# Kernel tuning notes

Hardware: AMD Instinct MI355X
Metric: run time of the kernel (lower is better)

Reference implementation:

```python
import jax, jax.numpy as jnp
import numpy as np

NUM_HEADS = 16

def setup_inputs() -> dict:
    key = jax.random.key(0)
    ks = jax.random.split(key, 8)
    B, S, D = 2, 2048, 1024
    H = NUM_HEADS
    s = 0.02
    return {
        "x": jax.random.normal(ks[0], (B, S, D), jnp.float32),
        "Wqkv": jax.random.normal(ks[1], (D, 3 * D), jnp.float32) * s,
        "bqkv": jnp.zeros((3 * D,), jnp.float32),
        "Wo": jax.random.normal(ks[2], (D, D), jnp.float32) * s,
        "bo": jnp.zeros((D,), jnp.float32),
        "mobius_scale": jnp.full((H,), 0.1, jnp.float32),
        "W1": jax.random.normal(ks[3], (D, D // 2), jnp.float32) * s,
        "b1": jnp.zeros((D // 2,), jnp.float32),
        "W2": jax.random.normal(ks[4], (D // 2, H), jnp.float32) * s,
        "b2": jnp.zeros((H,), jnp.float32),
        "adaptive_weight": jnp.full((1,), 0.1, jnp.float32),
    }

def reference(x, Wqkv, bqkv, Wo, bo, mobius_scale, W1, b1, W2, b2, adaptive_weight):
    B, S, D = x.shape
    H = NUM_HEADS
    dh = D // H
    # --- adaptive gating MLP on pooled context ---
    context = jnp.mean(x, axis=1, keepdims=True)                      # (B,1,D)
    h = jax.nn.gelu(context @ W1 + b1, approximate=False)             # (B,1,D/2)
    adaptive_factors = jax.nn.sigmoid(h @ W2 + b2)                    # (B,1,H)
    # --- incidence attention with mobius term ---
    qkv = (x @ Wqkv + bqkv).reshape(B, S, 3, H, dh)
    q, k, v = qkv[:, :, 0], qkv[:, :, 1], qkv[:, :, 2]                # (B,S,H,dh)
    scores = jnp.einsum("bshd,bthd->bhst", q, k) / jnp.sqrt(jnp.float32(dh))
    # Mobius map of the raw scores, learnable per-head scale
    scores = scores + mobius_scale[None, :, None, None] * (scores / (1.0 + scores * scores))
    attn = jax.nn.softmax(scores, axis=-1)                            # (B,H,S,S)
    out = jnp.einsum("bhst,bthd->bshd", attn, v).reshape(B, S, D)
    base_output = out @ Wo + bo                                       # (B,S,D)
    # --- training-path elementwise rescale ---
    adjustment = jnp.mean(adaptive_factors, axis=-1, keepdims=True)   # (B,1,1)
    return base_output * (1.0 + adaptive_weight * adjustment)
```

## Files before the change

kernel.cpp:

```cpp
#include <hip/hip_runtime.h>
#include <hip/hip_bf16.h>
#include <stdint.h>

typedef unsigned short u16;
typedef unsigned int u32;
typedef __attribute__((ext_vector_type(8))) short short8;
typedef __attribute__((ext_vector_type(4))) float f32x4;
typedef __attribute__((ext_vector_type(2))) float f32x2;
typedef __attribute__((ext_vector_type(4))) unsigned short u16x4;
typedef __attribute__((ext_vector_type(2))) unsigned int u32x2;

#define DEVFN static __device__ __forceinline__


DEVFN u16 f2bf(float f) {
  u32 u = __float_as_uint(f);
  u = (u + 0x7FFFu + ((u >> 16) & 1u)) >> 16;
  return (u16)u;
}

DEVFN u32 cvtpk_bf16(float lo, float hi) {
  u32 r;
  asm("v_cvt_pk_bf16_f32 %0, %1, %2" : "=v"(r) : "v"(lo), "v"(hi));
  return r;
}

DEVFN void gll16(const void* g, void* l) {
  __builtin_amdgcn_global_load_lds((const __attribute__((address_space(1))) u32*)g,
                                   (__attribute__((address_space(3))) u32*)l, 16, 0, 0);
}


__global__ void ctx_partial_kernel(const float* __restrict__ x, float* __restrict__ ctx) {
  int blk = blockIdx.x;
  int b = blk >> 7;
  int s0 = (blk & 127) * 16;
  int t = threadIdx.x;
  const float* xb = x + (size_t)b * 2048 * 1024 + (size_t)s0 * 1024;
#pragma unroll
  for (int c = 0; c < 4; ++c) {
    int d = c * 256 + t;
    float sum = 0.f;
#pragma unroll
    for (int s = 0; s < 16; ++s) sum += xb[(size_t)s * 1024 + d];
    atomicAdd(&ctx[b * 1024 + d], sum);
  }
}

__global__ void adaptive1_kernel(const float* __restrict__ ctx, const float* __restrict__ W1,
                                 const float* __restrict__ b1, float* __restrict__ hbuf) {
  int b = blockIdx.x >> 3, jb = blockIdx.x & 7;
  int t = threadIdx.x;
  int j = jb * 64 + (t & 63);
  int part = t >> 6;
  __shared__ float ctxs[1024];
  __shared__ float partial[4][64];
  for (int i = t; i < 1024; i += 256) ctxs[i] = ctx[b * 1024 + i] * (1.0f / 2048.0f);
  __syncthreads();
  float a0 = 0.f, a1 = 0.f;
  int d0 = part * 256;
  for (int d = d0; d < d0 + 256; d += 2) {
    a0 += ctxs[d] * W1[(size_t)d * 512 + j];
    a1 += ctxs[d + 1] * W1[(size_t)(d + 1) * 512 + j];
  }
  partial[part][t & 63] = a0 + a1;
  __syncthreads();
  if (t < 64) {
    float acc = b1[j] + ((partial[0][t] + partial[1][t]) + (partial[2][t] + partial[3][t]));
    hbuf[b * 512 + j] = 0.5f * acc * (1.0f + erff(acc * 0.70710678118654752f));
  }
}

__global__ void adaptive2_kernel(const float* __restrict__ hbuf, const float* __restrict__ W2,
                                 const float* __restrict__ b2, const float* __restrict__ aw,
                                 float* __restrict__ scale) {
  int b = blockIdx.x;
  int t = threadIdx.x;
  __shared__ float part[256];
  int o = t & 15, seg = t >> 4;
  float a = 0.f;
  for (int j = seg * 32; j < seg * 32 + 32; ++j) a += hbuf[b * 512 + j] * W2[(size_t)j * 16 + o];
  part[t] = a;
  __syncthreads();
  if (t < 16) {
    float acc = b2[t];
    for (int s2 = 0; s2 < 16; ++s2) acc += part[s2 * 16 + t];
    part[t] = 1.0f / (1.0f + __expf(-acc));
  }
  __syncthreads();
  if (t == 0) {
    float s = 0.f;
    for (int i = 0; i < 16; ++i) s += part[i];
    scale[b] = 1.0f + aw[0] * (s * (1.0f / 16.0f));
  }
}


__global__ void cvt_bf16_kernel(const float* __restrict__ in, u16* __restrict__ out, int n4) {
  int i = blockIdx.x * blockDim.x + threadIdx.x;
  if (i < n4) {
    float4 v = ((const float4*)in)[i];
    u16x4 o = {f2bf(v.x), f2bf(v.y), f2bf(v.z), f2bf(v.w)};
    ((u16x4*)out)[i] = o;
  }
}

__global__ void transpose_bf16_kernel(const float* __restrict__ in, u16* __restrict__ out,
                                      int K, int N) {
  __shared__ u16 tile[32][33];
  int n0 = blockIdx.x * 32, k0 = blockIdx.y * 32;
  int tc = threadIdx.x & 31, tr = threadIdx.x >> 5;
  for (int i = tr; i < 32; i += 8)
    tile[i][tc] = f2bf(in[(size_t)(k0 + i) * N + n0 + tc]);
  __syncthreads();
  for (int i = tr; i < 32; i += 8)
    out[(size_t)(n0 + i) * K + k0 + tc] = tile[tc][i];
}


DEVFN void gemm_tile_mainloop(const u16* __restrict__ A, const u16* __restrict__ Bt,
                              int m0, int n0, int K, u16* As, u16* Bs, f32x4 acc[4][4]) {
  const int tid = threadIdx.x;
  const int lane = tid & 63, wid = tid >> 6;
  const int wr = wid >> 1, wc = wid & 1;
  const int lr = lane & 15, lg = lane >> 4;
  const int srow = tid >> 2;
  const int scol = ((tid & 3) ^ ((tid >> 3) & 3)) * 8;
  const int axor = ((lr >> 1) & 3) << 4;

  const u16* ag0 = A + (size_t)(m0 + srow) * K + scol;
  const u16* ag1 = ag0 + (size_t)64 * K;
  const u16* bg0 = Bt + (size_t)(n0 + srow) * K + scol;
  const u16* bg1 = bg0 + (size_t)64 * K;

  gll16(ag0, As + tid * 8);
  gll16(ag1, As + (tid + 256) * 8);
  gll16(bg0, Bs + tid * 8);
  gll16(bg1, Bs + (tid + 256) * 8);

  int cur = 0;
  for (int k0 = 0; k0 < K; k0 += 32) {
    __syncthreads();
    if (k0 + 32 < K) {
      int nb = (cur ^ 1) * 4096;
      gll16(ag0 + k0 + 32, As + nb + tid * 8);
      gll16(ag1 + k0 + 32, As + nb + (tid + 256) * 8);
      gll16(bg0 + k0 + 32, Bs + nb + tid * 8);
      gll16(bg1 + k0 + 32, Bs + nb + (tid + 256) * 8);
    }
    const char* Ac = (const char*)(As + cur * 4096);
    const char* Bc = (const char*)(Bs + cur * 4096);
    short8 af[4], bf[4];
#pragma unroll
    for (int i = 0; i < 4; ++i)
      af[i] = *(const short8*)(Ac + (wr * 64 + i * 16 + lr) * 64 + ((lg * 16) ^ axor));
#pragma unroll
    for (int j = 0; j < 4; ++j)
      bf[j] = *(const short8*)(Bc + (wc * 64 + j * 16 + lr) * 64 + ((lg * 16) ^ axor));
#pragma unroll
    for (int i = 0; i < 4; ++i)
#pragma unroll
      for (int j = 0; j < 4; ++j)
        acc[i][j] = __builtin_amdgcn_mfma_f32_16x16x32_bf16(af[i], bf[j], acc[i][j], 0, 0, 0);
    cur ^= 1;
  }
}

DEVFN void gemm64_mainloop(const u16* __restrict__ A, const u16* __restrict__ Bt,
                           int m0, int n0, int K, u16* As, u16* Bs, f32x4 acc[2][2]) {
  const int tid = threadIdx.x;
  const int lane = tid & 63, wid = tid >> 6;
  const int wr = wid >> 1, wc = wid & 1;
  const int lr = lane & 15, lg = lane >> 4;
  const int srow = tid >> 2;
  const int scol = ((tid & 3) ^ ((tid >> 3) & 3)) * 8;
  const int axor = ((lr >> 1) & 3) << 4;

  const u16* ag = A + (size_t)(m0 + srow) * K + scol;
  const u16* bg = Bt + (size_t)(n0 + srow) * K + scol;
  gll16(ag, As + tid * 8);
  gll16(bg, Bs + tid * 8);

  int cur = 0;
  for (int k0 = 0; k0 < K; k0 += 32) {
    __syncthreads();
    if (k0 + 32 < K) {
      int nb = (cur ^ 1) * 2048;
      gll16(ag + k0 + 32, As + nb + tid * 8);
      gll16(bg + k0 + 32, Bs + nb + tid * 8);
    }
    const char* Ac = (const char*)(As + cur * 2048);
    const char* Bc = (const char*)(Bs + cur * 2048);
    short8 af[2], bf[2];
#pragma unroll
    for (int i = 0; i < 2; ++i)
      af[i] = *(const short8*)(Ac + (wr * 32 + i * 16 + lr) * 64 + ((lg * 16) ^ axor));
#pragma unroll
    for (int j = 0; j < 2; ++j)
      bf[j] = *(const short8*)(Bc + (wc * 32 + j * 16 + lr) * 64 + ((lg * 16) ^ axor));
#pragma unroll
    for (int i = 0; i < 2; ++i)
#pragma unroll
      for (int j = 0; j < 2; ++j)
        acc[i][j] = __builtin_amdgcn_mfma_f32_16x16x32_bf16(af[i], bf[j], acc[i][j], 0, 0, 0);
    cur ^= 1;
  }
}

__global__ __launch_bounds__(256) void gemm_qkv_kernel(
    const u16* __restrict__ A, const u16* __restrict__ Bt, const float* __restrict__ bias,
    u16* __restrict__ Qb, u16* __restrict__ Kb, u16* __restrict__ Vt) {
  __shared__ __align__(16) u16 As[2 * 128 * 32];
  __shared__ __align__(16) u16 Bs[2 * 128 * 32];
  f32x4 acc[4][4];
  const f32x4 z = {0.f, 0.f, 0.f, 0.f};
#pragma unroll
  for (int i = 0; i < 4; ++i)
#pragma unroll
    for (int j = 0; j < 4; ++j) acc[i][j] = z;
  int m0 = blockIdx.y * 128, n0 = blockIdx.x * 128;
  gemm_tile_mainloop(A, Bt, m0, n0, 1024, As, Bs, acc);

  const int lane = threadIdx.x & 63, wid = threadIdx.x >> 6;
  const int wr = wid >> 1, wc = wid & 1, lr = lane & 15, lg = lane >> 4;
#pragma unroll
  for (int j = 0; j < 4; ++j) {
    int col = n0 + wc * 64 + j * 16 + lr;
    float bv = bias[col];
    int c3 = col >> 10;
    int hh = (col >> 6) & 15, dd = col & 63;
    float qs = (c3 == 0) ? 0.125f : 1.0f;
#pragma unroll
    for (int i = 0; i < 4; ++i) {
      int row0 = m0 + wr * 64 + i * 16 + lg * 4;
      if (c3 == 2) {
        int b = row0 >> 11, s0 = row0 & 2047;
        u16x4 pv = {f2bf(acc[i][j][0] + bv), f2bf(acc[i][j][1] + bv),
                    f2bf(acc[i][j][2] + bv), f2bf(acc[i][j][3] + bv)};
        *(u16x4*)&Vt[(((size_t)b * 16 + hh) * 64 + dd) * 2048 + s0] = pv;
      } else {
        u16* dst = (c3 == 0) ? Qb : Kb;
#pragma unroll
        for (int r = 0; r < 4; ++r)
          dst[(size_t)(row0 + r) * 1024 + (col & 1023)] = f2bf((acc[i][j][r] + bv) * qs);
      }
    }
  }
}

__global__ __launch_bounds__(256) void gemm_out_kernel(
    const u16* __restrict__ A, const u16* __restrict__ Bt, const float* __restrict__ bo,
    const float* __restrict__ scale, float* __restrict__ out) {
  __shared__ __align__(16) u16 As[2 * 64 * 32];
  __shared__ __align__(16) u16 Bs[2 * 64 * 32];
  f32x4 acc[2][2];
  const f32x4 z = {0.f, 0.f, 0.f, 0.f};
#pragma unroll
  for (int i = 0; i < 2; ++i)
#pragma unroll
    for (int j = 0; j < 2; ++j) acc[i][j] = z;
  int m0 = blockIdx.y * 64, n0 = blockIdx.x * 64;
  gemm64_mainloop(A, Bt, m0, n0, 1024, As, Bs, acc);

  const int lane = threadIdx.x & 63, wid = threadIdx.x >> 6;
  const int wr = wid >> 1, wc = wid & 1, lr = lane & 15, lg = lane >> 4;
#pragma unroll
  for (int j = 0; j < 2; ++j) {
    int col = n0 + wc * 32 + j * 16 + lr;
    float bv = bo[col];
#pragma unroll
    for (int i = 0; i < 2; ++i) {
      int row0 = m0 + wr * 32 + i * 16 + lg * 4;
      float sc = scale[row0 >> 11];
#pragma unroll
      for (int r = 0; r < 4; ++r)
        out[(size_t)(row0 + r) * 1024 + col] = (acc[i][j][r] + bv) * sc;
    }
  }
}

__global__ __launch_bounds__(256) void attn_kernel(
    const u16* __restrict__ Qb, const u16* __restrict__ Kb, const u16* __restrict__ Vt,
    const float* __restrict__ mobius, u16* __restrict__ O) {
  __shared__ __align__(16) u16 Ks[2][64 * 64];
  __shared__ __align__(16) u16 Vs[2][64 * 64];
  __shared__ __align__(16) u16 Ps[64 * 64];
  const int tid = threadIdx.x;
  const int lane = tid & 63, w = tid >> 6;
  const int lr = lane & 15, lg = lane >> 4;
  const int bid = blockIdx.x;
  const int bidx = (bid & 7) * 128 + (bid >> 3);
  const int qb = bidx & 31, h = (bidx >> 5) & 15, b = bidx >> 9;
  const float msc = mobius[h];

  const int srow = tid >> 3;
  const int scol = ((tid & 7) ^ (srow & 7)) * 8;
  const int rxor = (lr & 7) << 4;

  const u16* qgl =
      Qb + (size_t)(b * 2048 + qb * 64 + w * 16 + lr) * 1024 + h * 64 + lg * 8;
  short8 qf0 = *(const short8*)qgl;
  short8 qf1 = *(const short8*)(qgl + 32);

  const u16* kg = Kb + (size_t)(b * 2048 + srow) * 1024 + h * 64 + scol;
  const u16* vg = Vt + ((size_t)(b * 16 + h) * 64 + srow) * 2048 + scol;

  gll16(kg, Ks[0] + tid * 8);
  gll16(kg + (size_t)32 * 1024, Ks[0] + (tid + 256) * 8);
  gll16(vg, Vs[0] + tid * 8);
  gll16(vg + 32 * 2048, Vs[0] + (tid + 256) * 8);

  float m_run = -3.0e38f, l_run = 0.0f;
  f32x4 acc_o[4];
  const f32x4 z = {0.f, 0.f, 0.f, 0.f};
#pragma unroll
  for (int i = 0; i < 4; ++i) acc_o[i] = z;

  const f32x2 one2 = {1.0f, 1.0f};
  const f32x2 msc2 = {msc, msc};
  const int qrow = w * 16 + lr;
  int cur = 0;
  for (int kt = 0; kt < 32; ++kt) {
    __syncthreads();
    if (kt < 31) {
      const u16* kgn = kg + (size_t)(kt + 1) * 64 * 1024;
      const u16* vgn = vg + (kt + 1) * 64;
      u16* Kn = Ks[cur ^ 1];
      u16* Vn = Vs[cur ^ 1];
      gll16(kgn, Kn + tid * 8);
      gll16(kgn + (size_t)32 * 1024, Kn + (tid + 256) * 8);
      gll16(vgn, Vn + tid * 8);
      gll16(vgn + 32 * 2048, Vn + (tid + 256) * 8);
    }
    const char* Kc = (const char*)Ks[cur];
    const char* Vc = (const char*)Vs[cur];
    const char* Pc = (const char*)Ps;

    f32x4 sacc[4];
#pragma unroll
    for (int i = 0; i < 4; ++i) sacc[i] = z;
    {
      int cbx = (lg * 16) ^ rxor;
#pragma unroll
      for (int ki = 0; ki < 4; ++ki) {
        short8 kf = *(const short8*)(Kc + (ki * 16 + lr) * 128 + cbx);
        sacc[ki] = __builtin_amdgcn_mfma_f32_16x16x32_bf16(kf, qf0, sacc[ki], 0, 0, 0);
      }
      cbx = (64 + lg * 16) ^ rxor;
#pragma unroll
      for (int ki = 0; ki < 4; ++ki) {
        short8 kf = *(const short8*)(Kc + (ki * 16 + lr) * 128 + cbx);
        sacc[ki] = __builtin_amdgcn_mfma_f32_16x16x32_bf16(kf, qf1, sacc[ki], 0, 0, 0);
      }
    }

    f32x2 p2[8];
    f32x2 mx = {-3.0e38f, -3.0e38f};
#pragma unroll
    for (int i = 0; i < 8; ++i) {
      int ki = i >> 1, jj = i & 1;
      f32x2 s = {sacc[ki][jj * 2], sacc[ki][jj * 2 + 1]};
      f32x2 d = s * s + one2;
      f32x2 rr = {__builtin_amdgcn_rcpf(d.x), __builtin_amdgcn_rcpf(d.y)};
      f32x2 t = msc2 * (s * rr) + s;
      p2[i] = t;
      mx = __builtin_elementwise_max(mx, t);
    }
    float tmax = fmaxf(mx.x, mx.y);
    tmax = fmaxf(tmax, __shfl_xor(tmax, 16));
    tmax = fmaxf(tmax, __shfl_xor(tmax, 32));
    float m_new = fmaxf(m_run, tmax);
    float corr = __expf(m_run - m_new);
    f32x2 m2 = {m_new, m_new};
    f32x2 sum2 = {0.f, 0.f};
#pragma unroll
    for (int i = 0; i < 8; ++i) {
      f32x2 e = p2[i] - m2;
      f32x2 pe = {__expf(e.x), __expf(e.y)};
      p2[i] = pe;
      sum2 += pe;
    }
    float tsum = sum2.x + sum2.y;
    tsum += __shfl_xor(tsum, 16);
    tsum += __shfl_xor(tsum, 32);
    l_run = l_run * corr + tsum;
    m_run = m_new;

#pragma unroll
    for (int ki = 0; ki < 4; ++ki) {
      u32x2 pw = {cvtpk_bf16(p2[2 * ki].x, p2[2 * ki].y),
                  cvtpk_bf16(p2[2 * ki + 1].x, p2[2 * ki + 1].y)};
      *(u32x2*)(Pc + qrow * 128 + ((ki * 32 + lg * 8) ^ rxor)) = pw;
    }

    float c4[4];
#pragma unroll
    for (int r = 0; r < 4; ++r) c4[r] = __shfl(corr, lg * 4 + r);
#pragma unroll
    for (int di = 0; di < 4; ++di)
#pragma unroll
      for (int r = 0; r < 4; ++r) acc_o[di][r] *= c4[r];

#pragma unroll
    for (int ks = 0; ks < 2; ++ks) {
      int cbx = (ks * 64 + lg * 16) ^ rxor;
      short8 pf = *(const short8*)(Pc + qrow * 128 + cbx);
#pragma unroll
      for (int di = 0; di < 4; ++di) {
        short8 vf = *(const short8*)(Vc + (di * 16 + lr) * 128 + cbx);
        acc_o[di] = __builtin_amdgcn_mfma_f32_16x16x32_bf16(pf, vf, acc_o[di], 0, 0, 0);
      }
    }
    cur ^= 1;
  }

  float linv = 1.0f / l_run;
  float li[4];
#pragma unroll
  for (int r = 0; r < 4; ++r) li[r] = __shfl(linv, lg * 4 + r);
  size_t obase = (size_t)(b * 2048 + qb * 64 + w * 16) * 1024 + h * 64;
#pragma unroll
  for (int di = 0; di < 4; ++di)
#pragma unroll
    for (int r = 0; r < 4; ++r)
      O[obase + (size_t)(lg * 4 + r) * 1024 + di * 16 + lr] = f2bf(acc_o[di][r] * li[r]);
}


extern "C" void kernel_launch(void* const* d_in, const int* in_sizes, int n_in,
                              void* d_out, int out_size, void* d_ws, size_t ws_size,
                              hipStream_t stream) {
  const float* x = (const float*)d_in[0];
  const float* Wqkv = (const float*)d_in[1];
  const float* bqkv = (const float*)d_in[2];
  const float* Wo = (const float*)d_in[3];
  const float* bo = (const float*)d_in[4];
  const float* mob = (const float*)d_in[5];
  const float* W1 = (const float*)d_in[6];
  const float* b1 = (const float*)d_in[7];
  const float* W2 = (const float*)d_in[8];
  const float* b2 = (const float*)d_in[9];
  const float* aw = (const float*)d_in[10];
  float* out = (float*)d_out;

  char* ws = (char*)d_ws;
  float* scale = (float*)ws;
  float* ctx = (float*)(ws + 256);
  float* hbuf = (float*)(ws + 8192);
  u16* xbf = (u16*)(ws + 16384);
  u16* wqkvT = xbf + (size_t)4096 * 1024;
  u16* woT = wqkvT + (size_t)3072 * 1024;
  u16* Qb = woT + (size_t)1024 * 1024;
  u16* Kb = Qb + (size_t)4096 * 1024;
  u16* Vt = Kb + (size_t)4096 * 1024;
  u16* attn = Vt + (size_t)4096 * 1024;

  hipMemsetAsync(ctx, 0, 2048 * sizeof(float), stream);
  ctx_partial_kernel<<<256, 256, 0, stream>>>(x, ctx);
  adaptive1_kernel<<<16, 256, 0, stream>>>(ctx, W1, b1, hbuf);
  adaptive2_kernel<<<2, 256, 0, stream>>>(hbuf, W2, b2, aw, scale);
  cvt_bf16_kernel<<<4096, 256, 0, stream>>>(x, xbf, 1048576);
  transpose_bf16_kernel<<<dim3(96, 32), 256, 0, stream>>>(Wqkv, wqkvT, 1024, 3072);
  transpose_bf16_kernel<<<dim3(32, 32), 256, 0, stream>>>(Wo, woT, 1024, 1024);
  gemm_qkv_kernel<<<dim3(24, 32), 256, 0, stream>>>(xbf, wqkvT, bqkv, Qb, Kb, Vt);
  attn_kernel<<<1024, 256, 0, stream>>>(Qb, Kb, Vt, mob, attn);
  gemm_out_kernel<<<dim3(16, 64), 256, 0, stream>>>(attn, woT, bo, scale, out);
}
```

Baseline: 272.4 us.

## Split attention over keys, fuse x conversion, swizzle GEMM grids, lazy softmax rescale

Attention is split into two key halves, doubling the grid, and a new combine kernel merges the two partial outputs using the saved per-row max and sum. V is read straight from global memory instead of being staged in LDS. The softmax now works in base 2, only rescales when the running max grows by more than a threshold, and raises wave priority around the MFMA sections. The mean-pooling and bf16 conversion of x are fused into one kernel. Both GEMMs get swizzled 1D grids and swapped MFMA operands so their epilogues can issue vectorised stores. The risks are the extra combine pass, the bf16 rounding of partial outputs before merging, and uncached V reads.

```diff
diff --git a/kernel.cpp b/kernel.cpp
--- a/kernel.cpp
+++ b/kernel.cpp
@@ -19,6 +19,8 @@
   return (u16)u;
 }
 
+DEVFN float bf2f(u16 v) { return __uint_as_float((u32)v << 16); }
+
 DEVFN u32 cvtpk_bf16(float lo, float hi) {
   u32 r;
   asm("v_cvt_pk_bf16_f32 %0, %1, %2" : "=v"(r) : "v"(lo), "v"(hi));
@@ -30,21 +32,30 @@
                                    (__attribute__((address_space(3))) u32*)l, 16, 0, 0);
 }
 
-
-__global__ void ctx_partial_kernel(const float* __restrict__ x, float* __restrict__ ctx) {
+__global__ void ctx_cvt_kernel(const float* __restrict__ x, float* __restrict__ ctx,
+                               u16* __restrict__ xbf) {
   int blk = blockIdx.x;
   int b = blk >> 7;
   int s0 = (blk & 127) * 16;
   int t = threadIdx.x;
-  const float* xb = x + (size_t)b * 2048 * 1024 + (size_t)s0 * 1024;
-#pragma unroll
-  for (int c = 0; c < 4; ++c) {
-    int d = c * 256 + t;
-    float sum = 0.f;
-#pragma unroll
-    for (int s = 0; s < 16; ++s) sum += xb[(size_t)s * 1024 + d];
-    atomicAdd(&ctx[b * 1024 + d], sum);
-  }
+  const float* xb = x + ((size_t)b * 2048 + s0) * 1024 + t * 4;
+  u16* ob = xbf + ((size_t)b * 2048 + s0) * 1024 + t * 4;
+  float4 sum = {0.f, 0.f, 0.f, 0.f};
+#pragma unroll
+  for (int s = 0; s < 16; ++s) {
+    float4 v = *(const float4*)(xb + (size_t)s * 1024);
+    sum.x += v.x;
+    sum.y += v.y;
+    sum.z += v.z;
+    sum.w += v.w;
+    u16x4 o = {f2bf(v.x), f2bf(v.y), f2bf(v.z), f2bf(v.w)};
+    *(u16x4*)(ob + (size_t)s * 1024) = o;
+  }
+  float* c = ctx + b * 1024 + t * 4;
+  atomicAdd(c + 0, sum.x);
+  atomicAdd(c + 1, sum.y);
+  atomicAdd(c + 2, sum.z);
+  atomicAdd(c + 3, sum.w);
 }
 
 __global__ void adaptive1_kernel(const float* __restrict__ ctx, const float* __restrict__ W1,
@@ -95,16 +106,6 @@
   }
 }
 
-
-__global__ void cvt_bf16_kernel(const float* __restrict__ in, u16* __restrict__ out, int n4) {
-  int i = blockIdx.x * blockDim.x + threadIdx.x;
-  if (i < n4) {
-    float4 v = ((const float4*)in)[i];
-    u16x4 o = {f2bf(v.x), f2bf(v.y), f2bf(v.z), f2bf(v.w)};
-    ((u16x4*)out)[i] = o;
-  }
-}
-
 __global__ void transpose_bf16_kernel(const float* __restrict__ in, u16* __restrict__ out,
                                       int K, int N) {
   __shared__ u16 tile[32][33];
@@ -161,7 +162,7 @@
     for (int i = 0; i < 4; ++i)
 #pragma unroll
       for (int j = 0; j < 4; ++j)
-        acc[i][j] = __builtin_amdgcn_mfma_f32_16x16x32_bf16(af[i], bf[j], acc[i][j], 0, 0, 0);
+        acc[i][j] = __builtin_amdgcn_mfma_f32_16x16x32_bf16(bf[j], af[i], acc[i][j], 0, 0, 0);
     cur ^= 1;
   }
 }
@@ -202,7 +203,7 @@
     for (int i = 0; i < 2; ++i)
 #pragma unroll
       for (int j = 0; j < 2; ++j)
-        acc[i][j] = __builtin_amdgcn_mfma_f32_16x16x32_bf16(af[i], bf[j], acc[i][j], 0, 0, 0);
+        acc[i][j] = __builtin_amdgcn_mfma_f32_16x16x32_bf16(bf[j], af[i], acc[i][j], 0, 0, 0);
     cur ^= 1;
   }
 }
@@ -218,31 +219,35 @@
   for (int i = 0; i < 4; ++i)
 #pragma unroll
     for (int j = 0; j < 4; ++j) acc[i][j] = z;
-  int m0 = blockIdx.y * 128, n0 = blockIdx.x * 128;
+  int lin = blockIdx.x;
+  int swz = (lin & 7) * 96 + (lin >> 3);
+  int n0 = (swz % 24) * 128, m0 = (swz / 24) * 128;
   gemm_tile_mainloop(A, Bt, m0, n0, 1024, As, Bs, acc);
 
   const int lane = threadIdx.x & 63, wid = threadIdx.x >> 6;
   const int wr = wid >> 1, wc = wid & 1, lr = lane & 15, lg = lane >> 4;
 #pragma unroll
-  for (int j = 0; j < 4; ++j) {
-    int col = n0 + wc * 64 + j * 16 + lr;
-    float bv = bias[col];
-    int c3 = col >> 10;
-    int hh = (col >> 6) & 15, dd = col & 63;
-    float qs = (c3 == 0) ? 0.125f : 1.0f;
-#pragma unroll
-    for (int i = 0; i < 4; ++i) {
-      int row0 = m0 + wr * 64 + i * 16 + lg * 4;
+  for (int i = 0; i < 4; ++i) {
+    int m = m0 + wr * 64 + i * 16 + lr;
+#pragma unroll
+    for (int j = 0; j < 4; ++j) {
+      int nb = n0 + wc * 64 + j * 16 + lg * 4;
+      float4 bv = *(const float4*)&bias[nb];
+      int c3 = nb >> 10;
       if (c3 == 2) {
-        int b = row0 >> 11, s0 = row0 & 2047;
-        u16x4 pv = {f2bf(acc[i][j][0] + bv), f2bf(acc[i][j][1] + bv),
-                    f2bf(acc[i][j][2] + bv), f2bf(acc[i][j][3] + bv)};
-        *(u16x4*)&Vt[(((size_t)b * 16 + hh) * 64 + dd) * 2048 + s0] = pv;
+        int bb = m >> 11, ss = m & 2047;
+        int hh = (nb >> 6) & 15, dd = nb & 63;
+        size_t vb_ = (((size_t)bb * 16 + hh) * 64 + dd) * 2048 + ss;
+        Vt[vb_] = f2bf(acc[i][j][0] + bv.x);
+        Vt[vb_ + 2048] = f2bf(acc[i][j][1] + bv.y);
+        Vt[vb_ + 4096] = f2bf(acc[i][j][2] + bv.z);
+        Vt[vb_ + 6144] = f2bf(acc[i][j][3] + bv.w);
       } else {
         u16* dst = (c3 == 0) ? Qb : Kb;
-#pragma unroll
-        for (int r = 0; r < 4; ++r)
-          dst[(size_t)(row0 + r) * 1024 + (col & 1023)] = f2bf((acc[i][j][r] + bv) * qs);
+        float qs = (c3 == 0) ? 0.125f : 1.0f;
+        u16x4 o = {f2bf((acc[i][j][0] + bv.x) * qs), f2bf((acc[i][j][1] + bv.y) * qs),
+                   f2bf((acc[i][j][2] + bv.z) * qs), f2bf((acc[i][j][3] + bv.w) * qs)};
+        *(u16x4*)&dst[(size_t)m * 1024 + (nb & 1023)] = o;
       }
     }
   }
@@ -259,56 +264,54 @@
   for (int i = 0; i < 2; ++i)
 #pragma unroll
     for (int j = 0; j < 2; ++j) acc[i][j] = z;
-  int m0 = blockIdx.y * 64, n0 = blockIdx.x * 64;
+  int lin = blockIdx.x;
+  int swz = (lin & 7) * 128 + (lin >> 3);
+  int n0 = (swz & 15) * 64, m0 = (swz >> 4) * 64;
   gemm64_mainloop(A, Bt, m0, n0, 1024, As, Bs, acc);
 
   const int lane = threadIdx.x & 63, wid = threadIdx.x >> 6;
   const int wr = wid >> 1, wc = wid & 1, lr = lane & 15, lg = lane >> 4;
 #pragma unroll
-  for (int j = 0; j < 2; ++j) {
-    int col = n0 + wc * 32 + j * 16 + lr;
-    float bv = bo[col];
-#pragma unroll
-    for (int i = 0; i < 2; ++i) {
-      int row0 = m0 + wr * 32 + i * 16 + lg * 4;
-      float sc = scale[row0 >> 11];
-#pragma unroll
-      for (int r = 0; r < 4; ++r)
-        out[(size_t)(row0 + r) * 1024 + col] = (acc[i][j][r] + bv) * sc;
-    }
-  }
-}
-
-__global__ __launch_bounds__(256) void attn_kernel(
+  for (int i = 0; i < 2; ++i) {
+    int m = m0 + wr * 32 + i * 16 + lr;
+    float sc = scale[m >> 11];
+#pragma unroll
+    for (int j = 0; j < 2; ++j) {
+      int nb = n0 + wc * 32 + j * 16 + lg * 4;
+      float4 bv = *(const float4*)&bo[nb];
+      float4 o = {(acc[i][j][0] + bv.x) * sc, (acc[i][j][1] + bv.y) * sc,
+                  (acc[i][j][2] + bv.z) * sc, (acc[i][j][3] + bv.w) * sc};
+      *(float4*)&out[(size_t)m * 1024 + nb] = o;
+    }
+  }
+}
+
+__global__ __launch_bounds__(256, 6) void attn_kernel(
     const u16* __restrict__ Qb, const u16* __restrict__ Kb, const u16* __restrict__ Vt,
-    const float* __restrict__ mobius, u16* __restrict__ O) {
+    const float* __restrict__ mobius, u16* __restrict__ O0, u16* __restrict__ O1,
+    float2* __restrict__ ML) {
   __shared__ __align__(16) u16 Ks[2][64 * 64];
-  __shared__ __align__(16) u16 Vs[2][64 * 64];
   __shared__ __align__(16) u16 Ps[64 * 64];
   const int tid = threadIdx.x;
   const int lane = tid & 63, w = tid >> 6;
   const int lr = lane & 15, lg = lane >> 4;
   const int bid = blockIdx.x;
-  const int bidx = (bid & 7) * 128 + (bid >> 3);
-  const int qb = bidx & 31, h = (bidx >> 5) & 15, b = bidx >> 9;
+  const int swz = (bid & 7) * 256 + (bid >> 3);
+  const int qb = swz & 31, h = (swz >> 5) & 15, b = (swz >> 9) & 1, spl = swz >> 10;
   const float msc = mobius[h];
 
   const int srow = tid >> 3;
   const int scol = ((tid & 7) ^ (srow & 7)) * 8;
   const int rxor = (lr & 7) << 4;
 
-  const u16* qgl =
-      Qb + (size_t)(b * 2048 + qb * 64 + w * 16 + lr) * 1024 + h * 64 + lg * 8;
+  const u16* qgl = Qb + (size_t)(b * 2048 + qb * 64 + w * 16 + lr) * 1024 + h * 64 + lg * 8;
   short8 qf0 = *(const short8*)qgl;
   short8 qf1 = *(const short8*)(qgl + 32);
 
-  const u16* kg = Kb + (size_t)(b * 2048 + srow) * 1024 + h * 64 + scol;
-  const u16* vg = Vt + ((size_t)(b * 16 + h) * 64 + srow) * 2048 + scol;
-
+  const u16* kg = Kb + ((size_t)(b * 2048 + spl * 1024 + srow)) * 1024 + h * 64 + scol;
+  const u16* vbase = Vt + ((size_t)(b * 16 + h) * 64) * 2048;
   gll16(kg, Ks[0] + tid * 8);
   gll16(kg + (size_t)32 * 1024, Ks[0] + (tid + 256) * 8);
-  gll16(vg, Vs[0] + tid * 8);
-  gll16(vg + 32 * 2048, Vs[0] + (tid + 256) * 8);
 
   float m_run = -3.0e38f, l_run = 0.0f;
   f32x4 acc_o[4];
@@ -316,29 +319,27 @@
 #pragma unroll
   for (int i = 0; i < 4; ++i) acc_o[i] = z;
 
+  const float L2E = 1.44269504f;
   const f32x2 one2 = {1.0f, 1.0f};
   const f32x2 msc2 = {msc, msc};
+  const f32x2 l2e2 = {L2E, L2E};
   const int qrow = w * 16 + lr;
+  const char* Pc = (const char*)Ps;
   int cur = 0;
-  for (int kt = 0; kt < 32; ++kt) {
+  for (int ktl = 0; ktl < 16; ++ktl) {
     __syncthreads();
-    if (kt < 31) {
-      const u16* kgn = kg + (size_t)(kt + 1) * 64 * 1024;
-      const u16* vgn = vg + (kt + 1) * 64;
+    if (ktl < 15) {
+      const u16* kgn = kg + (size_t)(ktl + 1) * 64 * 1024;
       u16* Kn = Ks[cur ^ 1];
-      u16* Vn = Vs[cur ^ 1];
       gll16(kgn, Kn + tid * 8);
       gll16(kgn + (size_t)32 * 1024, Kn + (tid + 256) * 8);
-      gll16(vgn, Vn + tid * 8);
-      gll16(vgn + 32 * 2048, Vn + (tid + 256) * 8);
     }
     const char* Kc = (const char*)Ks[cur];
-    const char* Vc = (const char*)Vs[cur];
-    const char* Pc = (const char*)Ps;
 
     f32x4 sacc[4];
 #pragma unroll
     for (int i = 0; i < 4; ++i) sacc[i] = z;
+    __builtin_amdgcn_s_setprio(1);
     {
       int cbx = (lg * 16) ^ rxor;
 #pragma unroll
@@ -353,6 +354,7 @@
         sacc[ki] = __builtin_amdgcn_mfma_f32_16x16x32_bf16(kf, qf1, sacc[ki], 0, 0, 0);
       }
     }
+    __builtin_amdgcn_s_setprio(0);
 
     f32x2 p2[8];
     f32x2 mx = {-3.0e38f, -3.0e38f};
@@ -362,29 +364,36 @@
       f32x2 s = {sacc[ki][jj * 2], sacc[ki][jj * 2 + 1]};
       f32x2 d = s * s + one2;
       f32x2 rr = {__builtin_amdgcn_rcpf(d.x), __builtin_amdgcn_rcpf(d.y)};
-      f32x2 t = msc2 * (s * rr) + s;
-      p2[i] = t;
-      mx = __builtin_elementwise_max(mx, t);
+      f32x2 tl = (msc2 * (s * rr) + s) * l2e2;
+      p2[i] = tl;
+      mx = __builtin_elementwise_max(mx, tl);
     }
     float tmax = fmaxf(mx.x, mx.y);
     tmax = fmaxf(tmax, __shfl_xor(tmax, 16));
     tmax = fmaxf(tmax, __shfl_xor(tmax, 32));
-    float m_new = fmaxf(m_run, tmax);
-    float corr = __expf(m_run - m_new);
-    f32x2 m2 = {m_new, m_new};
+    if (__any(tmax > m_run + 8.0f)) {
+      float m_new = fmaxf(m_run, tmax);
+      float corr = __builtin_amdgcn_exp2f(m_run - m_new);
+      m_run = m_new;
+      l_run *= corr;
+#pragma unroll
+      for (int di = 0; di < 4; ++di)
+#pragma unroll
+        for (int r = 0; r < 4; ++r) acc_o[di][r] *= corr;
+    }
+    f32x2 m2 = {m_run, m_run};
     f32x2 sum2 = {0.f, 0.f};
 #pragma unroll
     for (int i = 0; i < 8; ++i) {
       f32x2 e = p2[i] - m2;
-      f32x2 pe = {__expf(e.x), __expf(e.y)};
+      f32x2 pe = {__builtin_amdgcn_exp2f(e.x), __builtin_amdgcn_exp2f(e.y)};
       p2[i] = pe;
       sum2 += pe;
     }
     float tsum = sum2.x + sum2.y;
     tsum += __shfl_xor(tsum, 16);
     tsum += __shfl_xor(tsum, 32);
-    l_run = l_run * corr + tsum;
-    m_run = m_new;
+    l_run += tsum;
 
 #pragma unroll
     for (int ki = 0; ki < 4; ++ki) {
@@ -393,37 +402,57 @@
       *(u32x2*)(Pc + qrow * 128 + ((ki * 32 + lg * 8) ^ rxor)) = pw;
     }
 
-    float c4[4];
-#pragma unroll
-    for (int r = 0; r < 4; ++r) c4[r] = __shfl(corr, lg * 4 + r);
-#pragma unroll
-    for (int di = 0; di < 4; ++di)
-#pragma unroll
-      for (int r = 0; r < 4; ++r) acc_o[di][r] *= c4[r];
-
+    const u16* vk = vbase + (size_t)(spl * 1024 + ktl * 64) + (size_t)lr * 2048 + lg * 8;
+    __builtin_amdgcn_s_setprio(1);
 #pragma unroll
     for (int ks = 0; ks < 2; ++ks) {
-      int cbx = (ks * 64 + lg * 16) ^ rxor;
-      short8 pf = *(const short8*)(Pc + qrow * 128 + cbx);
+      short8 pf = *(const short8*)(Pc + qrow * 128 + ((ks * 64 + lg * 16) ^ rxor));
 #pragma unroll
       for (int di = 0; di < 4; ++di) {
-        short8 vf = *(const short8*)(Vc + (di * 16 + lr) * 128 + cbx);
-        acc_o[di] = __builtin_amdgcn_mfma_f32_16x16x32_bf16(pf, vf, acc_o[di], 0, 0, 0);
+        short8 vf = *(const short8*)(vk + (size_t)di * 16 * 2048 + ks * 32);
+        acc_o[di] = __builtin_amdgcn_mfma_f32_16x16x32_bf16(vf, pf, acc_o[di], 0, 0, 0);
       }
     }
+    __builtin_amdgcn_s_setprio(0);
     cur ^= 1;
   }
 
-  float linv = 1.0f / l_run;
-  float li[4];
-#pragma unroll
-  for (int r = 0; r < 4; ++r) li[r] = __shfl(linv, lg * 4 + r);
-  size_t obase = (size_t)(b * 2048 + qb * 64 + w * 16) * 1024 + h * 64;
-#pragma unroll
-  for (int di = 0; di < 4; ++di)
-#pragma unroll
-    for (int r = 0; r < 4; ++r)
-      O[obase + (size_t)(lg * 4 + r) * 1024 + di * 16 + lr] = f2bf(acc_o[di][r] * li[r]);
+  u16* Op = spl ? O1 : O0;
+  size_t obase = ((size_t)(b * 2048 + qb * 64 + w * 16 + lr)) * 1024 + h * 64;
+#pragma unroll
+  for (int di = 0; di < 4; ++di) {
+    u16x4 o = {f2bf(acc_o[di][0]), f2bf(acc_o[di][1]), f2bf(acc_o[di][2]), f2bf(acc_o[di][3])};
+    *(u16x4*)&Op[obase + di * 16 + lg * 4] = o;
+  }
+  if (lane < 16) {
+    float2 ml;
+    ml.x = m_run;
+    ml.y = l_run;
+    ML[(((size_t)spl * 2 + b) * 16 + h) * 2048 + qb * 64 + w * 16 + lane] = ml;
+  }
+}
+
+__global__ void attn_combine_kernel(const u16* __restrict__ O0, u16* __restrict__ O1,
+                                    const float2* __restrict__ ML) {
+  int e = blockIdx.x * 256 + threadIdx.x;
+  int dq = e & 15;
+  int h = (e >> 4) & 15;
+  int q = (e >> 8) & 2047;
+  int b = e >> 19;
+  float2 ml0 = ML[(((size_t)0 + b) * 16 + h) * 2048 + q];
+  float2 ml1 = ML[(((size_t)2 + b) * 16 + h) * 2048 + q];
+  float m = fmaxf(ml0.x, ml1.x);
+  float a0 = __builtin_amdgcn_exp2f(ml0.x - m);
+  float a1 = __builtin_amdgcn_exp2f(ml1.x - m);
+  float linv = 1.0f / (ml0.y * a0 + ml1.y * a1);
+  size_t off = ((size_t)b * 2048 + q) * 1024 + h * 64 + dq * 4;
+  u16x4 v0 = *(const u16x4*)&O0[off];
+  u16x4 v1 = *(const u16x4*)&O1[off];
+  u16x4 o;
+#pragma unroll
+  for (int j = 0; j < 4; ++j)
+    o[j] = f2bf((bf2f(v0[j]) * a0 + bf2f(v1[j]) * a1) * linv);
+  *(u16x4*)&O1[off] = o;
 }
 
 
@@ -443,26 +472,30 @@
   const float* aw = (const float*)d_in[10];
   float* out = (float*)d_out;
 
+  const size_t MB = 1024 * 1024;
   char* ws = (char*)d_ws;
   float* scale = (float*)ws;
   float* ctx = (float*)(ws + 256);
-  float* hbuf = (float*)(ws + 8192);
-  u16* xbf = (u16*)(ws + 16384);
-  u16* wqkvT = xbf + (size_t)4096 * 1024;
-  u16* woT = wqkvT + (size_t)3072 * 1024;
-  u16* Qb = woT + (size_t)1024 * 1024;
-  u16* Kb = Qb + (size_t)4096 * 1024;
-  u16* Vt = Kb + (size_t)4096 * 1024;
-  u16* attn = Vt + (size_t)4096 * 1024;
+  float* hbuf = (float*)(ws + 16384);
+  char* base = ws + 32768;
+  u16* xbf = (u16*)base;
+  u16* wqkvT = (u16*)(base + 8 * MB);
+  u16* woT = (u16*)(base + 14 * MB);
+  u16* Qb = (u16*)(base + 16 * MB);
+  u16* Kb = (u16*)(base + 24 * MB);
+  u16* Vt = (u16*)(base + 32 * MB);
+  u16* attn = (u16*)(base + 40 * MB);
+  u16* O0 = xbf;
+  float2* ML = (float2*)wqkvT;
 
   hipMemsetAsync(ctx, 0, 2048 * sizeof(float), stream);
-  ctx_partial_kernel<<<256, 256, 0, stream>>>(x, ctx);
+  ctx_cvt_kernel<<<256, 256, 0, stream>>>(x, ctx, xbf);
   adaptive1_kernel<<<16, 256, 0, stream>>>(ctx, W1, b1, hbuf);
   adaptive2_kernel<<<2, 256, 0, stream>>>(hbuf, W2, b2, aw, scale);
-  cvt_bf16_kernel<<<4096, 256, 0, stream>>>(x, xbf, 1048576);
   transpose_bf16_kernel<<<dim3(96, 32), 256, 0, stream>>>(Wqkv, wqkvT, 1024, 3072);
   transpose_bf16_kernel<<<dim3(32, 32), 256, 0, stream>>>(Wo, woT, 1024, 1024);
-  gemm_qkv_kernel<<<dim3(24, 32), 256, 0, stream>>>(xbf, wqkvT, bqkv, Qb, Kb, Vt);
-  attn_kernel<<<1024, 256, 0, stream>>>(Qb, Kb, Vt, mob, attn);
-  gemm_out_kernel<<<dim3(16, 64), 256, 0, stream>>>(attn, woT, bo, scale, out);
-}
+  gemm_qkv_kernel<<<768, 256, 0, stream>>>(xbf, wqkvT, bqkv, Qb, Kb, Vt);
+  attn_kernel<<<2048, 256, 0, stream>>>(Qb, Kb, Vt, mob, O0, attn, ML);
+  attn_combine_kernel<<<4096, 256, 0, stream>>>(O0, attn, ML);
+  gemm_out_kernel<<<1024, 256, 0, stream>>>(attn, woT, bo, scale, out);
+}
```

Result: slower. 341.4 us (+25.3%).
